# Performance work log

Measured on AMD Instinct MI355X. Metric: run time of the kernel, lower is better.

## Reference

```python
import jax, jax.numpy as jnp
import numpy as np

R, N, F, H, C = 3, 100000, 256, 128, 2
N0, S1, D1, S2, D2 = 16384, 16384, 4096, 4096, 512


def setup_inputs() -> dict:
    key = jax.random.key(0)
    ks = jax.random.split(key, 13)
    return {
        "features": jax.random.normal(ks[0], (N, F), jnp.float32),
        "src_nodes": jax.random.randint(ks[1], (R, N0), 0, N),
        "dstsrc2src1": jax.random.randint(ks[2], (R, S1), 0, N0),
        "dstsrc2dst1": jax.random.randint(ks[3], (R, D1), 0, N0),
        "dif_mat1": jax.random.uniform(ks[4], (R, D1, S1), jnp.float32) / S1,
        "dstsrc2src2": jax.random.randint(ks[5], (R, S2), 0, D1),
        "dstsrc2dst2": jax.random.randint(ks[6], (R, D2), 0, D1),
        "dif_mat2": jax.random.uniform(ks[7], (R, D2, S2), jnp.float32) / S2,
        "w1": jax.random.normal(ks[8], (2 * F, H), jnp.float32) * 0.05,
        "w2": jax.random.normal(ks[9], (2 * H, H), jnp.float32) * 0.05,
        "relation_vectors": jax.random.uniform(ks[10], (R, H), jnp.float32),
        "attention_vec": jax.random.uniform(ks[11], (2 * H, 1), jnp.float32),
        "classifier_w": jax.random.normal(ks[12], (H, C), jnp.float32) * 0.05,
    }


def _agg(x, d2s, d2d, dif, w, rel_vec, att_vec):
    # x: [n, din]; dif: [d, s]; w: [2*din, H]
    agg = dif @ x[d2s]                                  # mean-diffused neighbor feats [d, din]
    h = jnp.concatenate([agg, x[d2d]], axis=1) @ w      # [d, H]
    rel = jnp.broadcast_to(rel_vec[None, :], (h.shape[0], rel_vec.shape[0]))
    score = (jnp.concatenate([h, rel], axis=1) @ att_vec)[:, 0]  # [d]
    att = jax.nn.softmax(score)                         # softmax over batch nodes
    return h * att[:, None]


def reference(features, src_nodes, dstsrc2src1, dstsrc2dst1, dif_mat1,
              dstsrc2src2, dstsrc2dst2, dif_mat2, w1, w2,
              relation_vectors, attention_vec, classifier_w):
    def per_relation(src, s1, d1, m1, s2, d2, m2, rel_vec):
        x = features[src]                               # gather node feats [N0, F]
        x = _agg(x, s1, d1, m1, w1, rel_vec, attention_vec)   # [D1, H]
        x = _agg(x, s2, d2, m2, w2, rel_vec, attention_vec)   # [D2, H]
        return x

    xs = jax.vmap(per_relation)(src_nodes, dstsrc2src1, dstsrc2dst1, dif_mat1,
                                dstsrc2src2, dstsrc2dst2, dif_mat2, relation_vectors)
    summed = jnp.sum(xs, axis=0)                        # sum over relations [D2, H]
    inv_norm = jax.lax.rsqrt(jnp.maximum(jnp.sum(summed * summed, axis=1, keepdims=True), 1e-12))
    normed = summed * inv_norm                          # tf.nn.l2_normalize(axis=1)
    return jax.nn.softmax(normed @ classifier_w, axis=-1)
```

## Files before the change

kernel.cpp:

```cpp
#include <hip/hip_runtime.h>
#include <hip/hip_bf16.h>
#include <math.h>

constexpr int Rc  = 3;
constexpr int Fc  = 256;
constexpr int Hc  = 128;
constexpr int N0c = 16384;
constexpr int S1c = 16384;
constexpr int D1c = 4096;
constexpr int S2c = 4096;
constexpr int D2c = 512;
constexpr int KH1 = 4;
constexpr int KH2 = 16;

typedef __bf16 bf16x8 __attribute__((ext_vector_type(8)));
typedef float  f32x4  __attribute__((ext_vector_type(4)));

__device__ __forceinline__ void glds16(const void* g, void* l) {
  __builtin_amdgcn_global_load_lds(
      (const __attribute__((address_space(1))) void*)g,
      (__attribute__((address_space(3))) void*)l, 16, 0, 0);
}

__device__ __forceinline__ bf16x8 cvt2(const float4 a, const float4 b) {
  bf16x8 c;
  c[0] = (__bf16)a.x; c[1] = (__bf16)a.y; c[2] = (__bf16)a.z; c[3] = (__bf16)a.w;
  c[4] = (__bf16)b.x; c[5] = (__bf16)b.y; c[6] = (__bf16)b.z; c[7] = (__bf16)b.w;
  return c;
}

__device__ __forceinline__ unsigned short bfbits(float v) {
  __bf16 b = (__bf16)v; unsigned short u;
  __builtin_memcpy(&u, &b, 2); return u;
}

__global__ __launch_bounds__(256, 2)
void wpack(const float* __restrict__ w1, const float* __restrict__ w2,
           unsigned char* __restrict__ wp, float* __restrict__ esum) {
  const int tile = blockIdx.x, half = blockIdx.y, t = threadIdx.x;
  if (tile == 0 && half == 0 && t < 8) esum[t] = 0.f;
  const float* src; int row0;
  if (tile < 4)       { src = w1; row0 = tile * 64; }
  else if (tile < 8)  { src = w1; row0 = 256 + (tile - 4) * 64; }
  else if (tile < 10) { src = w2; row0 = (tile - 8) * 64; }
  else                { src = w2; row0 = 128 + (tile - 10) * 64; }
  unsigned char* dst = wp + ((size_t)half * 12 + tile) * 16384;
  __shared__ float sm[64][132];
  {
    const int r = t >> 2, c0 = (t & 3) * 32;
#pragma unroll
    for (int j = 0; j < 8; j++)
      *(float4*)&sm[r][c0 + 4 * j] = *(const float4*)(src + (size_t)(row0 + r) * 128 + c0 + 4 * j);
  }
  __syncthreads();
  if (t < 128) {
    const int n = t;
#pragma unroll
    for (int ch = 0; ch < 8; ch++) {
      bf16x8 o;
#pragma unroll
      for (int e = 0; e < 8; e++) {
        float v = sm[ch * 8 + e][n];
        __bf16 h = (__bf16)v;
        o[e] = half ? (__bf16)(v - (float)h) : h;
      }
      *(bf16x8*)(dst + n * 128 + ((ch ^ (n & 7)) * 16)) = o;
    }
  }
}

__global__ __launch_bounds__(256, 3)
void gg_layer1(const float* __restrict__ feat, const int* __restrict__ srcn,
               const int* __restrict__ d2s1, const int* __restrict__ d2d1,
               const unsigned char* __restrict__ wp,
               unsigned char* __restrict__ xgwp, float* __restrict__ xdw) {
  const int rel = blockIdx.y;
  int bx = blockIdx.x;
  const int job = bx >= 256 ? 1 : 0;
  if (job) bx -= 256;
  const int s0 = bx * 64;
  const int rows = job ? D1c : S1c;
  const int* idx = job ? d2d1 : d2s1;
  const unsigned char* Bh = wp + (size_t)(job ? 4 : 0) * 16384;
  const unsigned char* Bl = wp + (size_t)(12 + (job ? 4 : 0)) * 16384;

  const int t = threadIdx.x, lane = t & 63, w = t >> 6;
  const int mh = w >> 1, nh = w & 1;

  __shared__ __bf16 Asm[64 * 64];
  __shared__ __bf16 Bhs[128 * 64];
  __shared__ __bf16 Bls[128 * 64];

  const int arow = t >> 2, ak0 = (t & 3) * 16;
  const int row = s0 + arow;
  const size_t arowg = (size_t)srcn[rel * N0c + idx[(size_t)rel * rows + row]];
  const float* aptr = feat + arowg * Fc + ak0;
  const int ac0 = ak0 >> 3;
  __bf16* asw0 = &Asm[arow * 64 + ((ac0    ) ^ (arow & 7)) * 8];
  __bf16* asw1 = &Asm[arow * 64 + ((ac0 + 1) ^ (arow & 7)) * 8];

  float4 a[16];
#pragma unroll
  for (int tl = 0; tl < 4; tl++)
#pragma unroll
    for (int j = 0; j < 4; j++) a[tl * 4 + j] = *(const float4*)(aptr + tl * 64 + 4 * j);

  f32x4 acc[2][4] = {};

  for (int tl = 0; tl < 4; ++tl) {
    asm volatile("s_waitcnt lgkmcnt(0)" ::: "memory");
    __builtin_amdgcn_s_barrier();
    __builtin_amdgcn_sched_barrier(0);
    {
      const unsigned char* bh = Bh + (size_t)tl * 16384 + w * 4096 + lane * 16;
      const unsigned char* bl = Bl + (size_t)tl * 16384 + w * 4096 + lane * 16;
      char* dh = (char*)Bhs + w * 4096;
      char* dl = (char*)Bls + w * 4096;
#pragma unroll
      for (int i = 0; i < 4; i++) glds16(bh + i * 1024, dh + i * 1024);
#pragma unroll
      for (int i = 0; i < 4; i++) glds16(bl + i * 1024, dl + i * 1024);
    }
    *(bf16x8*)asw0 = cvt2(a[tl * 4 + 0], a[tl * 4 + 1]);
    *(bf16x8*)asw1 = cvt2(a[tl * 4 + 2], a[tl * 4 + 3]);
    asm volatile("s_waitcnt vmcnt(0) lgkmcnt(0)" ::: "memory");
    __builtin_amdgcn_s_barrier();
    __builtin_amdgcn_sched_barrier(0);
#pragma unroll
    for (int ks = 0; ks < 2; ks++) {
      const int ch = ks * 4 + (lane >> 4);
      bf16x8 af[2], bh[4], bl[4];
#pragma unroll
      for (int mi = 0; mi < 2; mi++) {
        int r = mh * 32 + mi * 16 + (lane & 15);
        af[mi] = *(const bf16x8*)&Asm[r * 64 + ((ch ^ (r & 7)) * 8)];
      }
#pragma unroll
      for (int ni = 0; ni < 4; ni++) {
        int n = nh * 64 + ni * 16 + (lane & 15);
        bh[ni] = *(const bf16x8*)&Bhs[n * 64 + ((ch ^ (n & 7)) * 8)];
        bl[ni] = *(const bf16x8*)&Bls[n * 64 + ((ch ^ (n & 7)) * 8)];
      }
#pragma unroll
      for (int mi = 0; mi < 2; mi++)
#pragma unroll
        for (int ni = 0; ni < 4; ni++) {
          acc[mi][ni] = __builtin_amdgcn_mfma_f32_16x16x32_bf16(af[mi], bh[ni], acc[mi][ni], 0, 0, 0);
          acc[mi][ni] = __builtin_amdgcn_mfma_f32_16x16x32_bf16(af[mi], bl[ni], acc[mi][ni], 0, 0, 0);
        }
    }
  }
  if (job) {
#pragma unroll
    for (int mi = 0; mi < 2; mi++)
#pragma unroll
      for (int ni = 0; ni < 4; ni++) {
        const int col = nh * 64 + ni * 16 + (lane & 15);
#pragma unroll
        for (int j = 0; j < 4; j++) {
          const int r = mh * 32 + mi * 16 + (lane >> 4) * 4 + j;
          xdw[((size_t)rel * D1c + s0 + r) * 128 + col] = acc[mi][ni][j];
        }
      }
  } else {
    unsigned char* tile = xgwp + ((size_t)(rel * (S1c >> 6) + bx)) * 16384;
#pragma unroll
    for (int mi = 0; mi < 2; mi++)
#pragma unroll
      for (int ni = 0; ni < 4; ni++) {
        const int sl0 = mh * 32 + mi * 16 + (lane >> 4) * 4;
        const int n = nh * 64 + ni * 16 + (lane & 15);
        const int ch = sl0 >> 3, e0 = sl0 & 7, cs = ch ^ (n & 7);
        ushort4 u;
        u.x = bfbits(acc[mi][ni][0]); u.y = bfbits(acc[mi][ni][1]);
        u.z = bfbits(acc[mi][ni][2]); u.w = bfbits(acc[mi][ni][3]);
        *(ushort4*)(tile + n * 128 + cs * 16 + e0 * 2) = u;
      }
  }
}

template <int SWZ>
__global__ __launch_bounds__(256, 3)
void gemm_big(const float* __restrict__ A, const unsigned char* __restrict__ Bp,
              float* __restrict__ C, int M, int KTOT, int KH) {
  int rel, kh, m0;
  if (SWZ) {
    const int F = blockIdx.x;
    const int xcd = F & 7, r = F >> 3;
    const int sub = r >> 5, m = r & 31;
    const int h = xcd + 8 * sub;
    const int g = h >> 1;
    rel = g >> 2; kh = g & 3;
    m0 = ((h & 1) * 32 + m) * 64;
  } else {
    rel = blockIdx.z; kh = blockIdx.y; m0 = blockIdx.x * 64;
  }
  const int t = threadIdx.x, lane = t & 63, w = t >> 6;
  const int KB = KTOT / KH, NT = KB >> 6;
  const int mh = w >> 1, nh = w & 1;

  const float* Ag = A + ((size_t)rel * M + m0) * KTOT + (size_t)kh * KB;
  const unsigned char* Bt = Bp + ((size_t)rel * (KTOT >> 6) + (size_t)kh * NT) * 16384;
  float* Cg = C + (((size_t)kh * Rc + rel) * M + m0) * 128;

  __shared__ __bf16 Asm[64 * 64];
  __shared__ __bf16 Bsm[2][128 * 64];

  f32x4 acc[2][4] = {};
  const int arow = t >> 2, ak0 = (t & 3) * 16;
  const float* aptr = Ag + (size_t)arow * KTOT + ak0;
  const int ac0 = ak0 >> 3;
  __bf16* asw0 = &Asm[arow * 64 + ((ac0    ) ^ (arow & 7)) * 8];
  __bf16* asw1 = &Asm[arow * 64 + ((ac0 + 1) ^ (arow & 7)) * 8];
  const unsigned char* bsrc = Bt + w * 4096 + lane * 16;

  float4 a0[4], a1[4];
#pragma unroll
  for (int j = 0; j < 4; j++) a0[j] = *(const float4*)(aptr + 4 * j);
  {
    char* bd = (char*)Bsm[0] + w * 4096;
#pragma unroll
    for (int i = 0; i < 4; i++) glds16(bsrc + i * 1024, bd + i * 1024);
  }

  for (int tl = 0; tl < NT; ++tl) {
    const int cur = tl & 1;
    asm volatile("s_waitcnt lgkmcnt(0)" ::: "memory");
    __builtin_amdgcn_s_barrier();
    __builtin_amdgcn_sched_barrier(0);
    if (tl + 1 < NT) {
      const unsigned char* bs = bsrc + (size_t)(tl + 1) * 16384;
      char* bd = (char*)Bsm[cur ^ 1] + w * 4096;
#pragma unroll
      for (int i = 0; i < 4; i++) glds16(bs + i * 1024, bd + i * 1024);
      const float* ap = aptr + (size_t)(tl + 1) * 64;
#pragma unroll
      for (int j = 0; j < 4; j++) a1[j] = *(const float4*)(ap + 4 * j);
    }
    *(bf16x8*)asw0 = cvt2(a0[0], a0[1]);
    *(bf16x8*)asw1 = cvt2(a0[2], a0[3]);
    if (tl + 1 < NT)
      asm volatile("s_waitcnt vmcnt(8) lgkmcnt(0)" ::: "memory");
    else
      asm volatile("s_waitcnt vmcnt(0) lgkmcnt(0)" ::: "memory");
    __builtin_amdgcn_s_barrier();
    __builtin_amdgcn_sched_barrier(0);
    const __bf16* Bc = Bsm[cur];
#pragma unroll
    for (int ks = 0; ks < 2; ks++) {
      const int ch = ks * 4 + (lane >> 4);
      bf16x8 af[2], bfr[4];
#pragma unroll
      for (int mi = 0; mi < 2; mi++) {
        int r = mh * 32 + mi * 16 + (lane & 15);
        af[mi] = *(const bf16x8*)&Asm[r * 64 + ((ch ^ (r & 7)) * 8)];
      }
#pragma unroll
      for (int ni = 0; ni < 4; ni++) {
        int n = nh * 64 + ni * 16 + (lane & 15);
        bfr[ni] = *(const bf16x8*)&Bc[n * 64 + ((ch ^ (n & 7)) * 8)];
      }
#pragma unroll
      for (int mi = 0; mi < 2; mi++)
#pragma unroll
        for (int ni = 0; ni < 4; ni++)
          acc[mi][ni] = __builtin_amdgcn_mfma_f32_16x16x32_bf16(af[mi], bfr[ni], acc[mi][ni], 0, 0, 0);
    }
#pragma unroll
    for (int j = 0; j < 4; j++) a0[j] = a1[j];
  }
#pragma unroll
  for (int mi = 0; mi < 2; mi++)
#pragma unroll
    for (int ni = 0; ni < 4; ni++) {
      const int col = nh * 64 + ni * 16 + (lane & 15);
#pragma unroll
      for (int j = 0; j < 4; j++) {
        const int r = mh * 32 + mi * 16 + (lane >> 4) * 4 + j;
        Cg[(size_t)r * 128 + col] = acc[mi][ni][j];
      }
    }
}

__global__ __launch_bounds__(256, 3)
void c1_l2(const float* __restrict__ aggP, const float* __restrict__ xdw,
           const float* __restrict__ attv, const unsigned char* __restrict__ wp,
           float* __restrict__ escore1, float* __restrict__ esum,
           float* __restrict__ P, float* __restrict__ Q) {
  const int rel = blockIdx.y, d0 = blockIdx.x * 64;
  const int t = threadIdx.x, lane = t & 63, w = t >> 6;
  const int mh = w >> 1, nh = w & 1;

  __shared__ __bf16 Asm[64 * 128];
  __shared__ __bf16 Bhs[128 * 64];
  __shared__ __bf16 Bls[128 * 64];
  __shared__ float  sred[64];

  const int r = t >> 2, c0 = (t & 3) * 32;
  float4 x0[8];
  {
    const size_t base = ((size_t)rel * D1c + d0 + r) * 128 + c0;
#pragma unroll
    for (int j = 0; j < 8; j++) x0[j] = *(const float4*)(xdw + base + 4 * j);
#pragma unroll
    for (int p2 = 0; p2 < KH1; p2++) {
      const float* ap = aggP + (((size_t)p2 * Rc + rel) * D1c + d0 + r) * 128 + c0;
#pragma unroll
      for (int j = 0; j < 8; j++) {
        float4 u = *(const float4*)(ap + 4 * j);
        x0[j].x += u.x; x0[j].y += u.y; x0[j].z += u.z; x0[j].w += u.w;
      }
    }
  }
  float sp = 0.f;
#pragma unroll
  for (int j = 0; j < 8; j++) {
    sp += x0[j].x * attv[c0 + 4 * j]     + x0[j].y * attv[c0 + 4 * j + 1]
        + x0[j].z * attv[c0 + 4 * j + 2] + x0[j].w * attv[c0 + 4 * j + 3];
  }
  sp += __shfl_xor(sp, 1); sp += __shfl_xor(sp, 2);
  const float e = expf(sp);
  if ((t & 3) == 0) { escore1[(size_t)rel * D1c + d0 + r] = e; sred[r] = e; }
  const int ch0 = (t & 3) * 4;
#pragma unroll
  for (int q = 0; q < 4; q++) {
    *(bf16x8*)&Asm[r * 128 + (((ch0 + q) ^ (r & 7)) * 8)] = cvt2(x0[2 * q], x0[2 * q + 1]);
  }
  __syncthreads();
  if (t < 64) {
    float v = sred[t];
    v += __shfl_down(v, 32); v += __shfl_down(v, 16); v += __shfl_down(v, 8);
    v += __shfl_down(v, 4);  v += __shfl_down(v, 2);  v += __shfl_down(v, 1);
    if (t == 0) atomicAdd(esum + rel, v);
  }
  f32x4 accP[2][4] = {}, accQ[2][4] = {};
#pragma unroll
  for (int z = 0; z < 2; z++) {
#pragma unroll
    for (int tl = 0; tl < 2; tl++) {
      if (!(z == 0 && tl == 0)) {
        asm volatile("s_waitcnt lgkmcnt(0)" ::: "memory");
        __builtin_amdgcn_s_barrier();
        __builtin_amdgcn_sched_barrier(0);
      }
      {
        const unsigned char* bh = wp + (size_t)(8 + z * 2 + tl) * 16384 + w * 4096 + lane * 16;
        const unsigned char* bl = wp + (size_t)(20 + z * 2 + tl) * 16384 + w * 4096 + lane * 16;
        char* dh = (char*)Bhs + w * 4096;
        char* dl = (char*)Bls + w * 4096;
#pragma unroll
        for (int i = 0; i < 4; i++) glds16(bh + i * 1024, dh + i * 1024);
#pragma unroll
        for (int i = 0; i < 4; i++) glds16(bl + i * 1024, dl + i * 1024);
      }
      asm volatile("s_waitcnt vmcnt(0) lgkmcnt(0)" ::: "memory");
      __builtin_amdgcn_s_barrier();
      __builtin_amdgcn_sched_barrier(0);
      f32x4 (*acc)[4] = z ? accQ : accP;
#pragma unroll
      for (int ks = 0; ks < 2; ks++) {
        const int lch = ks * 4 + (lane >> 4);
        const int ch  = tl * 8 + lch;
        bf16x8 af[2], bh[4], bl[4];
#pragma unroll
        for (int mi = 0; mi < 2; mi++) {
          int rr = mh * 32 + mi * 16 + (lane & 15);
          af[mi] = *(const bf16x8*)&Asm[rr * 128 + ((ch ^ (rr & 7)) * 8)];
        }
#pragma unroll
        for (int ni = 0; ni < 4; ni++) {
          int n = nh * 64 + ni * 16 + (lane & 15);
          bh[ni] = *(const bf16x8*)&Bhs[n * 64 + ((lch ^ (n & 7)) * 8)];
          bl[ni] = *(const bf16x8*)&Bls[n * 64 + ((lch ^ (n & 7)) * 8)];
        }
#pragma unroll
        for (int mi = 0; mi < 2; mi++)
#pragma unroll
          for (int ni = 0; ni < 4; ni++) {
            acc[mi][ni] = __builtin_amdgcn_mfma_f32_16x16x32_bf16(af[mi], bh[ni], acc[mi][ni], 0, 0, 0);
            acc[mi][ni] = __builtin_amdgcn_mfma_f32_16x16x32_bf16(af[mi], bl[ni], acc[mi][ni], 0, 0, 0);
          }
      }
    }
  }
#pragma unroll
  for (int mi = 0; mi < 2; mi++)
#pragma unroll
    for (int ni = 0; ni < 4; ni++) {
      const int col = nh * 64 + ni * 16 + (lane & 15);
#pragma unroll
      for (int j = 0; j < 4; j++) {
        const int rr = mh * 32 + mi * 16 + (lane >> 4) * 4 + j;
        P[((size_t)rel * D1c + d0 + rr) * 128 + col] = accP[mi][ni][j];
        Q[((size_t)rel * D1c + d0 + rr) * 128 + col] = accQ[mi][ni][j];
      }
    }
}

__global__ __launch_bounds__(256, 2)
void pgpack(const float* __restrict__ P, const int* __restrict__ d2s2,
            const float* __restrict__ escore1, const float* __restrict__ esum,
            unsigned char* __restrict__ PGp) {
  const int rel = blockIdx.y, kb = blockIdx.x, t = threadIdx.x;
  const float inv1 = 1.0f / esum[rel];
  __shared__ __bf16 sm[64][136];
  {
    const int kl = t >> 2, c0 = (t & 3) * 32;
    const int sr = d2s2[rel * S2c + kb * 64 + kl];
    const float sc = escore1[(size_t)rel * D1c + sr] * inv1;
    const float4* p = (const float4*)(P + ((size_t)rel * D1c + sr) * 128 + c0);
#pragma unroll
    for (int j = 0; j < 4; j++) {
      float4 v0 = p[2 * j], v1 = p[2 * j + 1];
      v0.x *= sc; v0.y *= sc; v0.z *= sc; v0.w *= sc;
      v1.x *= sc; v1.y *= sc; v1.z *= sc; v1.w *= sc;
      *(bf16x8*)&sm[kl][c0 + 8 * j] = cvt2(v0, v1);
    }
  }
  __syncthreads();
  if (t < 128) {
    const int n = t;
    unsigned char* dst = PGp + ((size_t)(rel * (S2c >> 6) + kb)) * 16384;
#pragma unroll
    for (int ch = 0; ch < 8; ch++) {
      bf16x8 o;
#pragma unroll
      for (int e = 0; e < 8; e++) o[e] = sm[ch * 8 + e][n];
      *(bf16x8*)(dst + n * 128 + ((ch ^ (n & 7)) * 16)) = o;
    }
  }
}

__global__ __launch_bounds__(128, 4)
void combine2(const float* __restrict__ aggP2, const float* __restrict__ Q,
              const int* __restrict__ d2d2, const float* __restrict__ attv,
              const float* __restrict__ escore1, const float* __restrict__ esum,
              float* __restrict__ h2, float* __restrict__ escore2) {
  const int rel = blockIdx.y, d0 = blockIdx.x * 8, t = threadIdx.x;
  const float inv1 = 1.0f / esum[rel];
  float acc[8];
#pragma unroll
  for (int i = 0; i < 8; i++) {
    const int d = d0 + i;
    const int qr = d2d2[rel * D2c + d];
    const float qs = escore1[(size_t)rel * D1c + qr] * inv1;
    float v = Q[((size_t)rel * D1c + qr) * 128 + t] * qs;
#pragma unroll
    for (int p = 0; p < KH2; p++)
      v += aggP2[(((size_t)p * Rc + rel) * D2c + d) * 128 + t];
    acc[i] = v;
    h2[((size_t)rel * D2c + d) * 128 + t] = v;
  }
  const float avt = attv[t];
  __shared__ float sred[2][8];
#pragma unroll
  for (int i = 0; i < 8; i++) {
    float p = acc[i] * avt;
    p += __shfl_down(p, 32); p += __shfl_down(p, 16); p += __shfl_down(p, 8);
    p += __shfl_down(p, 4);  p += __shfl_down(p, 2);  p += __shfl_down(p, 1);
    if ((t & 63) == 0) sred[t >> 6][i] = p;
  }
  __syncthreads();
  if (t < 8) {
    const float e2 = expf(sred[0][t] + sred[1][t]);
    escore2[rel * D2c + d0 + t] = e2;
    float v = e2;
    v += __shfl_down(v, 4); v += __shfl_down(v, 2); v += __shfl_down(v, 1);
    if (t == 0) atomicAdd((float*)esum + 4 + rel, v);
  }
}

__global__ __launch_bounds__(128, 4)
void k9_final(const float* __restrict__ h2, const float* __restrict__ escore2,
              const float* __restrict__ esum, const float* __restrict__ cw,
              float* __restrict__ out) {
  const int d = blockIdx.x, t = threadIdx.x;
  float v = 0.f;
#pragma unroll
  for (int r = 0; r < Rc; r++) {
    const float att = escore2[r * D2c + d] / esum[4 + r];
    v += h2[((size_t)r * D2c + d) * Hc + t] * att;
  }
  float ss = v * v;
  ss += __shfl_down(ss, 32); ss += __shfl_down(ss, 16); ss += __shfl_down(ss, 8);
  ss += __shfl_down(ss, 4);  ss += __shfl_down(ss, 2);  ss += __shfl_down(ss, 1);
  __shared__ float sr[3][2];
  if ((t & 63) == 0) sr[0][t >> 6] = ss;
  __syncthreads();
  const float tot = sr[0][0] + sr[0][1];
  const float inv = rsqrtf(fmaxf(tot, 1e-12f));
  const float nv = v * inv;
  float p0 = nv * cw[t * 2], p1 = nv * cw[t * 2 + 1];
  p0 += __shfl_down(p0, 32); p0 += __shfl_down(p0, 16); p0 += __shfl_down(p0, 8);
  p0 += __shfl_down(p0, 4);  p0 += __shfl_down(p0, 2);  p0 += __shfl_down(p0, 1);
  p1 += __shfl_down(p1, 32); p1 += __shfl_down(p1, 16); p1 += __shfl_down(p1, 8);
  p1 += __shfl_down(p1, 4);  p1 += __shfl_down(p1, 2);  p1 += __shfl_down(p1, 1);
  if ((t & 63) == 0) { sr[1][t >> 6] = p0; sr[2][t >> 6] = p1; }
  __syncthreads();
  if (t == 0) {
    const float l0 = sr[1][0] + sr[1][1];
    const float l1 = sr[2][0] + sr[2][1];
    const float m = fmaxf(l0, l1);
    const float e0 = expf(l0 - m), e1 = expf(l1 - m);
    const float is = 1.0f / (e0 + e1);
    out[d * 2 + 0] = e0 * is;
    out[d * 2 + 1] = e1 * is;
  }
}

extern "C" void kernel_launch(void* const* d_in, const int* in_sizes, int n_in,
                              void* d_out, int out_size, void* d_ws, size_t ws_size,
                              hipStream_t stream) {
  (void)in_sizes; (void)n_in; (void)out_size; (void)ws_size;
  const float* feat = (const float*)d_in[0];
  const int*   srcn = (const int*)d_in[1];
  const int*   d2s1 = (const int*)d_in[2];
  const int*   d2d1 = (const int*)d_in[3];
  const float* dif1 = (const float*)d_in[4];
  const int*   d2s2 = (const int*)d_in[5];
  const int*   d2d2 = (const int*)d_in[6];
  const float* dif2 = (const float*)d_in[7];
  const float* w1   = (const float*)d_in[8];
  const float* w2   = (const float*)d_in[9];
  const float* attv = (const float*)d_in[11];
  const float* cw   = (const float*)d_in[12];
  float* out = (float*)d_out;

  char* p = (char*)d_ws;
  auto take = [&](size_t n) { char* r = p; p += (n + 255) & ~(size_t)255; return r; };
  unsigned char* wp   = (unsigned char*)take(24 * 16384);
  unsigned char* xgwp = (unsigned char*)take((size_t)Rc * 256 * 16384);
  float* xdw    = (float*)take((size_t)Rc * D1c * 128 * 4);
  float* aggP   = (float*)take((size_t)KH1 * Rc * D1c * 128 * 4);
  float* escore1= (float*)take((size_t)Rc * D1c * 4);
  float* esum   = (float*)take(256);
  unsigned char* PGp = (unsigned char*)take((size_t)Rc * 64 * 16384);
  float* h2     = (float*)take((size_t)Rc * D2c * 128 * 4);
  float* escore2= (float*)take((size_t)Rc * D2c * 4);
  float* P = (float*)xgwp;
  float* Q = P + (size_t)Rc * D1c * 128;
  float* aggP2 = aggP;

  wpack<<<dim3(12, 2), 256, 0, stream>>>(w1, w2, wp, esum);
  gg_layer1<<<dim3(320, Rc), 256, 0, stream>>>(feat, srcn, d2s1, d2d1, wp, xgwp, xdw);
  gemm_big<1><<<768, 256, 0, stream>>>(dif1, xgwp, aggP, D1c, S1c, KH1);
  c1_l2<<<dim3(D1c / 64, Rc), 256, 0, stream>>>(aggP, xdw, attv, wp, escore1, esum, P, Q);
  pgpack<<<dim3(S2c / 64, Rc), 256, 0, stream>>>(P, d2s2, escore1, esum, PGp);
  gemm_big<0><<<dim3(D2c / 64, KH2, Rc), 256, 0, stream>>>(dif2, PGp, aggP2, D2c, S2c, KH2);
  combine2<<<dim3(D2c / 8, Rc), 128, 0, stream>>>(aggP2, Q, d2d2, attv, escore1, esum, h2, escore2);
  k9_final<<<D2c, 128, 0, stream>>>(h2, escore2, esum, cw, out);
}
```

Measured before the change: 284.9 us.

## Move d2d1 gather-GEMM job into the big dif1 GEMM launch

The dst-side gather-and-project work (xdw) is split out of the layer-1 gather kernel and appended as 192 extra blocks to a specialized copy of the big dif1 GEMM kernel. The first kernel now handles only the src-side tiles. This shortens the critical path of the first kernel and lets the independent xdw work fill idle slots alongside the large GEMM. The GEMM part is specialized with compile-time tile counts and shares a union LDS buffer with the second path, which can change occupancy and register pressure.

```diff
diff --git a/kernel.cpp b/kernel.cpp
--- a/kernel.cpp
+++ b/kernel.cpp
@@ -70,19 +70,12 @@
 }
 
 __global__ __launch_bounds__(256, 3)
-void gg_layer1(const float* __restrict__ feat, const int* __restrict__ srcn,
-               const int* __restrict__ d2s1, const int* __restrict__ d2d1,
-               const unsigned char* __restrict__ wp,
-               unsigned char* __restrict__ xgwp, float* __restrict__ xdw) {
-  const int rel = blockIdx.y;
-  int bx = blockIdx.x;
-  const int job = bx >= 256 ? 1 : 0;
-  if (job) bx -= 256;
-  const int s0 = bx * 64;
-  const int rows = job ? D1c : S1c;
-  const int* idx = job ? d2d1 : d2s1;
-  const unsigned char* Bh = wp + (size_t)(job ? 4 : 0) * 16384;
-  const unsigned char* Bl = wp + (size_t)(12 + (job ? 4 : 0)) * 16384;
+void gg0(const float* __restrict__ feat, const int* __restrict__ srcn,
+         const int* __restrict__ d2s1, const unsigned char* __restrict__ wp,
+         unsigned char* __restrict__ xgwp) {
+  const int rel = blockIdx.y, bx = blockIdx.x, s0 = bx * 64;
+  const unsigned char* Bh = wp;
+  const unsigned char* Bl = wp + (size_t)12 * 16384;
 
   const int t = threadIdx.x, lane = t & 63, w = t >> 6;
   const int mh = w >> 1, nh = w & 1;
@@ -93,7 +86,7 @@
 
   const int arow = t >> 2, ak0 = (t & 3) * 16;
   const int row = s0 + arow;
-  const size_t arowg = (size_t)srcn[rel * N0c + idx[(size_t)rel * rows + row]];
+  const size_t arowg = (size_t)srcn[rel * N0c + d2s1[(size_t)rel * S1c + row]];
   const float* aptr = feat + arowg * Fc + ak0;
   const int ac0 = ak0 >> 3;
   __bf16* asw0 = &Asm[arow * 64 + ((ac0    ) ^ (arow & 7)) * 8];
@@ -150,51 +143,212 @@
         }
     }
   }
-  if (job) {
-#pragma unroll
-    for (int mi = 0; mi < 2; mi++)
-#pragma unroll
-      for (int ni = 0; ni < 4; ni++) {
-        const int col = nh * 64 + ni * 16 + (lane & 15);
-#pragma unroll
-        for (int j = 0; j < 4; j++) {
-          const int r = mh * 32 + mi * 16 + (lane >> 4) * 4 + j;
-          xdw[((size_t)rel * D1c + s0 + r) * 128 + col] = acc[mi][ni][j];
-        }
-      }
-  } else {
-    unsigned char* tile = xgwp + ((size_t)(rel * (S1c >> 6) + bx)) * 16384;
-#pragma unroll
-    for (int mi = 0; mi < 2; mi++)
-#pragma unroll
-      for (int ni = 0; ni < 4; ni++) {
-        const int sl0 = mh * 32 + mi * 16 + (lane >> 4) * 4;
-        const int n = nh * 64 + ni * 16 + (lane & 15);
-        const int ch = sl0 >> 3, e0 = sl0 & 7, cs = ch ^ (n & 7);
-        ushort4 u;
-        u.x = bfbits(acc[mi][ni][0]); u.y = bfbits(acc[mi][ni][1]);
-        u.z = bfbits(acc[mi][ni][2]); u.w = bfbits(acc[mi][ni][3]);
-        *(ushort4*)(tile + n * 128 + cs * 16 + e0 * 2) = u;
-      }
-  }
-}
-
-template <int SWZ>
+  unsigned char* tile = xgwp + ((size_t)(rel * (S1c >> 6) + bx)) * 16384;
+#pragma unroll
+  for (int mi = 0; mi < 2; mi++)
+#pragma unroll
+    for (int ni = 0; ni < 4; ni++) {
+      const int sl0 = mh * 32 + mi * 16 + (lane >> 4) * 4;
+      const int n = nh * 64 + ni * 16 + (lane & 15);
+      const int ch = sl0 >> 3, e0 = sl0 & 7, cs = ch ^ (n & 7);
+      ushort4 u;
+      u.x = bfbits(acc[mi][ni][0]); u.y = bfbits(acc[mi][ni][1]);
+      u.z = bfbits(acc[mi][ni][2]); u.w = bfbits(acc[mi][ni][3]);
+      *(ushort4*)(tile + n * 128 + cs * 16 + e0 * 2) = u;
+    }
+}
+
 __global__ __launch_bounds__(256, 3)
-void gemm_big(const float* __restrict__ A, const unsigned char* __restrict__ Bp,
-              float* __restrict__ C, int M, int KTOT, int KH) {
-  int rel, kh, m0;
-  if (SWZ) {
+void big1p(const float* __restrict__ dif1, const unsigned char* __restrict__ xgwp,
+           float* __restrict__ aggP, const float* __restrict__ feat,
+           const int* __restrict__ srcn, const int* __restrict__ d2d1,
+           const unsigned char* __restrict__ wp, float* __restrict__ xdw) {
+  __shared__ char lds[40960];
+  const int t = threadIdx.x, lane = t & 63, w = t >> 6;
+  const int mh = w >> 1, nh = w & 1;
+
+  if (blockIdx.x < 768) {
+    __bf16* Asm  = (__bf16*)lds;
+    __bf16* Bsm0 = (__bf16*)(lds + 8192);
+    __bf16* Bsm1 = (__bf16*)(lds + 24576);
     const int F = blockIdx.x;
     const int xcd = F & 7, r = F >> 3;
     const int sub = r >> 5, m = r & 31;
     const int h = xcd + 8 * sub;
     const int g = h >> 1;
-    rel = g >> 2; kh = g & 3;
-    m0 = ((h & 1) * 32 + m) * 64;
+    const int rel = g >> 2, kh = g & 3;
+    const int m0 = ((h & 1) * 32 + m) * 64;
+    constexpr int NT = 64;
+
+    const float* Ag = dif1 + ((size_t)rel * D1c + m0) * S1c + (size_t)kh * 4096;
+    const unsigned char* Bt = xgwp + ((size_t)rel * 256 + (size_t)kh * NT) * 16384;
+    float* Cg = aggP + (((size_t)kh * Rc + rel) * D1c + m0) * 128;
+
+    f32x4 acc[2][4] = {};
+    const int arow = t >> 2, ak0 = (t & 3) * 16;
+    const float* aptr = Ag + (size_t)arow * S1c + ak0;
+    const int ac0 = ak0 >> 3;
+    __bf16* asw0 = &Asm[arow * 64 + ((ac0    ) ^ (arow & 7)) * 8];
+    __bf16* asw1 = &Asm[arow * 64 + ((ac0 + 1) ^ (arow & 7)) * 8];
+    const unsigned char* bsrc = Bt + w * 4096 + lane * 16;
+
+    float4 a0[4], a1[4], a2[4];
+    {
+      char* bd = (char*)Bsm0 + w * 4096;
+#pragma unroll
+      for (int i = 0; i < 4; i++) glds16(bsrc + i * 1024, bd + i * 1024);
+    }
+#pragma unroll
+    for (int j = 0; j < 4; j++) a0[j] = *(const float4*)(aptr + 4 * j);
+#pragma unroll
+    for (int j = 0; j < 4; j++) a1[j] = *(const float4*)(aptr + 64 + 4 * j);
+
+    for (int tl = 0; tl < NT; ++tl) {
+      __bf16* Bc = (tl & 1) ? Bsm1 : Bsm0;
+      __bf16* Bn = (tl & 1) ? Bsm0 : Bsm1;
+      asm volatile("s_waitcnt lgkmcnt(0)" ::: "memory");
+      __builtin_amdgcn_s_barrier();
+      __builtin_amdgcn_sched_barrier(0);
+      if (tl + 1 < NT) {
+        const unsigned char* bs = bsrc + (size_t)(tl + 1) * 16384;
+        char* bd = (char*)Bn + w * 4096;
+#pragma unroll
+        for (int i = 0; i < 4; i++) glds16(bs + i * 1024, bd + i * 1024);
+      }
+      if (tl + 2 < NT) {
+        const float* ap = aptr + (size_t)(tl + 2) * 64;
+#pragma unroll
+        for (int j = 0; j < 4; j++) a2[j] = *(const float4*)(ap + 4 * j);
+      }
+      *(bf16x8*)asw0 = cvt2(a0[0], a0[1]);
+      *(bf16x8*)asw1 = cvt2(a0[2], a0[3]);
+      if (tl + 2 < NT)
+        asm volatile("s_waitcnt vmcnt(12) lgkmcnt(0)" ::: "memory");
+      else if (tl + 1 < NT)
+        asm volatile("s_waitcnt vmcnt(8) lgkmcnt(0)" ::: "memory");
+      else
+        asm volatile("s_waitcnt vmcnt(0) lgkmcnt(0)" ::: "memory");
+      __builtin_amdgcn_s_barrier();
+      __builtin_amdgcn_sched_barrier(0);
+#pragma unroll
+      for (int ks = 0; ks < 2; ks++) {
+        const int ch = ks * 4 + (lane >> 4);
+        bf16x8 af[2], bfr[4];
+#pragma unroll
+        for (int mi = 0; mi < 2; mi++) {
+          int rr = mh * 32 + mi * 16 + (lane & 15);
+          af[mi] = *(const bf16x8*)&Asm[rr * 64 + ((ch ^ (rr & 7)) * 8)];
+        }
+#pragma unroll
+        for (int ni = 0; ni < 4; ni++) {
+          int n = nh * 64 + ni * 16 + (lane & 15);
+          bfr[ni] = *(const bf16x8*)&Bc[n * 64 + ((ch ^ (n & 7)) * 8)];
+        }
+#pragma unroll
+        for (int mi = 0; mi < 2; mi++)
+#pragma unroll
+          for (int ni = 0; ni < 4; ni++)
+            acc[mi][ni] = __builtin_amdgcn_mfma_f32_16x16x32_bf16(af[mi], bfr[ni], acc[mi][ni], 0, 0, 0);
+      }
+#pragma unroll
+      for (int j = 0; j < 4; j++) { a0[j] = a1[j]; a1[j] = a2[j]; }
+    }
+#pragma unroll
+    for (int mi = 0; mi < 2; mi++)
+#pragma unroll
+      for (int ni = 0; ni < 4; ni++) {
+        const int col = nh * 64 + ni * 16 + (lane & 15);
+#pragma unroll
+        for (int j = 0; j < 4; j++) {
+          const int rr = mh * 32 + mi * 16 + (lane >> 4) * 4 + j;
+          Cg[(size_t)rr * 128 + col] = acc[mi][ni][j];
+        }
+      }
   } else {
-    rel = blockIdx.z; kh = blockIdx.y; m0 = blockIdx.x * 64;
-  }
+    __bf16* Asm = (__bf16*)lds;
+    __bf16* Bhs = (__bf16*)(lds + 8192);
+    __bf16* Bls = (__bf16*)(lds + 24576);
+    const int jb = blockIdx.x - 768;
+    const int rel = jb >> 6, bx = jb & 63, s0 = bx * 64;
+    const unsigned char* Bh = wp + (size_t)4 * 16384;
+    const unsigned char* Bl = wp + (size_t)16 * 16384;
+
+    const int arow = t >> 2, ak0 = (t & 3) * 16;
+    const int row = s0 + arow;
+    const size_t arowg = (size_t)srcn[rel * N0c + d2d1[(size_t)rel * D1c + row]];
+    const float* aptr = feat + arowg * Fc + ak0;
+    const int ac0 = ak0 >> 3;
+    __bf16* asw0 = &Asm[arow * 64 + ((ac0    ) ^ (arow & 7)) * 8];
+    __bf16* asw1 = &Asm[arow * 64 + ((ac0 + 1) ^ (arow & 7)) * 8];
+
+    float4 a[16];
+#pragma unroll
+    for (int tl = 0; tl < 4; tl++)
+#pragma unroll
+      for (int j = 0; j < 4; j++) a[tl * 4 + j] = *(const float4*)(aptr + tl * 64 + 4 * j);
+
+    f32x4 acc[2][4] = {};
+    for (int tl = 0; tl < 4; ++tl) {
+      asm volatile("s_waitcnt lgkmcnt(0)" ::: "memory");
+      __builtin_amdgcn_s_barrier();
+      __builtin_amdgcn_sched_barrier(0);
+      {
+        const unsigned char* bh = Bh + (size_t)tl * 16384 + w * 4096 + lane * 16;
+        const unsigned char* bl = Bl + (size_t)tl * 16384 + w * 4096 + lane * 16;
+        char* dh = (char*)Bhs + w * 4096;
+        char* dl = (char*)Bls + w * 4096;
+#pragma unroll
+        for (int i = 0; i < 4; i++) glds16(bh + i * 1024, dh + i * 1024);
+#pragma unroll
+        for (int i = 0; i < 4; i++) glds16(bl + i * 1024, dl + i * 1024);
+      }
+      *(bf16x8*)asw0 = cvt2(a[tl * 4 + 0], a[tl * 4 + 1]);
+      *(bf16x8*)asw1 = cvt2(a[tl * 4 + 2], a[tl * 4 + 3]);
+      asm volatile("s_waitcnt vmcnt(0) lgkmcnt(0)" ::: "memory");
+      __builtin_amdgcn_s_barrier();
+      __builtin_amdgcn_sched_barrier(0);
+#pragma unroll
+      for (int ks = 0; ks < 2; ks++) {
+        const int ch = ks * 4 + (lane >> 4);
+        bf16x8 af[2], bh[4], bl[4];
+#pragma unroll
+        for (int mi = 0; mi < 2; mi++) {
+          int r = mh * 32 + mi * 16 + (lane & 15);
+          af[mi] = *(const bf16x8*)&Asm[r * 64 + ((ch ^ (r & 7)) * 8)];
+        }
+#pragma unroll
+        for (int ni = 0; ni < 4; ni++) {
+          int n = nh * 64 + ni * 16 + (lane & 15);
+          bh[ni] = *(const bf16x8*)&Bhs[n * 64 + ((ch ^ (n & 7)) * 8)];
+          bl[ni] = *(const bf16x8*)&Bls[n * 64 + ((ch ^ (n & 7)) * 8)];
+        }
+#pragma unroll
+        for (int mi = 0; mi < 2; mi++)
+#pragma unroll
+          for (int ni = 0; ni < 4; ni++) {
+            acc[mi][ni] = __builtin_amdgcn_mfma_f32_16x16x32_bf16(af[mi], bh[ni], acc[mi][ni], 0, 0, 0);
+            acc[mi][ni] = __builtin_amdgcn_mfma_f32_16x16x32_bf16(af[mi], bl[ni], acc[mi][ni], 0, 0, 0);
+          }
+      }
+    }
+#pragma unroll
+    for (int mi = 0; mi < 2; mi++)
+#pragma unroll
+      for (int ni = 0; ni < 4; ni++) {
+        const int col = nh * 64 + ni * 16 + (lane & 15);
+#pragma unroll
+        for (int j = 0; j < 4; j++) {
+          const int rr = mh * 32 + mi * 16 + (lane >> 4) * 4 + j;
+          xdw[((size_t)rel * D1c + s0 + rr) * 128 + col] = acc[mi][ni][j];
+        }
+      }
+  }
+}
+
+__global__ __launch_bounds__(256, 3)
+void gemm_big(const float* __restrict__ A, const unsigned char* __restrict__ Bp,
+              float* __restrict__ C, int M, int KTOT, int KH) {
+  const int rel = blockIdx.z, kh = blockIdx.y, m0 = blockIdx.x * 64;
   const int t = threadIdx.x, lane = t & 63, w = t >> 6;
   const int KB = KTOT / KH, NT = KB >> 6;
   const int mh = w >> 1, nh = w & 1;
@@ -542,11 +696,11 @@
   float* aggP2 = aggP;
 
   wpack<<<dim3(12, 2), 256, 0, stream>>>(w1, w2, wp, esum);
-  gg_layer1<<<dim3(320, Rc), 256, 0, stream>>>(feat, srcn, d2s1, d2d1, wp, xgwp, xdw);
-  gemm_big<1><<<768, 256, 0, stream>>>(dif1, xgwp, aggP, D1c, S1c, KH1);
+  gg0<<<dim3(256, Rc), 256, 0, stream>>>(feat, srcn, d2s1, wp, xgwp);
+  big1p<<<960, 256, 0, stream>>>(dif1, xgwp, aggP, feat, srcn, d2d1, wp, xdw);
   c1_l2<<<dim3(D1c / 64, Rc), 256, 0, stream>>>(aggP, xdw, attv, wp, escore1, esum, P, Q);
   pgpack<<<dim3(S2c / 64, Rc), 256, 0, stream>>>(P, d2s2, escore1, esum, PGp);
-  gemm_big<0><<<dim3(D2c / 64, KH2, Rc), 256, 0, stream>>>(dif2, PGp, aggP2, D2c, S2c, KH2);
+  gemm_big<<<dim3(D2c / 64, KH2, Rc), 256, 0, stream>>>(dif2, PGp, aggP2, D2c, S2c, KH2);
   combine2<<<dim3(D2c / 8, Rc), 128, 0, stream>>>(aggP2, Q, d2d2, attv, escore1, esum, h2, escore2);
   k9_final<<<D2c, 128, 0, stream>>>(h2, escore2, esum, cw, out);
 }
```

Result: no change. 286.0 us (+0.4%).
